# Optimization experiments

Measured on AMD Instinct MI355X. Metric: run time of the kernel, lower is better.

## Reference

```python
import jax, jax.numpy as jnp
import numpy as np

LMAX = 10
BATCH = 16384


def _pairs():
    return [(l1, l2) for l1 in range(LMAX + 1) for l2 in range(l1, LMAX + 1)]


def _cg_offsets():
    # flat-buffer offset and coupled dimension d=(2l1+1)(2l2+1) per (l1,l2) pair
    offs = {}
    off = 0
    for (l1, l2) in _pairs():
        d = (2 * l1 + 1) * (2 * l2 + 1)
        offs[(l1, l2)] = (off, d)
        off += d * d
    return offs, off


def _full_coeffs(coeffs):
    # coeffs: (B, LMAX+1, LMAX+1) complex, entry [:, l, m] holds f_{l,m} for m>=0.
    # Real-signal symmetry: f_{l,-m} = (-1)^m conj(f_{l,m}).
    f = {}
    for l in range(LMAX + 1):
        pos = coeffs[:, l, : l + 1]  # m = 0..l
        if l == 0:
            f[l] = pos
        else:
            mm = np.arange(l, 0, -1)  # |m| for m = -l..-1
            sign = jnp.asarray(((-1.0) ** mm), dtype=jnp.float32)
            neg = sign * jnp.conj(coeffs[:, l, 1 : l + 1][:, ::-1])
            f[l] = jnp.concatenate([neg, pos], axis=1)  # (B, 2l+1), m = -l..l
    return f


def setup_inputs() -> dict:
    key = jax.random.key(0)
    k1, k2, k3 = jax.random.split(key, 3)
    _, total = _cg_offsets()
    return {
        "coeffs_re": jax.random.normal(k1, (BATCH, LMAX + 1, LMAX + 1), dtype=jnp.float32),
        "coeffs_im": jax.random.normal(k2, (BATCH, LMAX + 1, LMAX + 1), dtype=jnp.float32),
        "cg_flat": jax.random.normal(k3, (total,), dtype=jnp.float32),
    }


def reference(coeffs_re, coeffs_im, cg_flat):
    coeffs = jax.lax.complex(coeffs_re, coeffs_im)  # (B, L+1, L+1) complex64
    f = _full_coeffs(coeffs)
    offs, _ = _cg_offsets()
    B = coeffs.shape[0]
    cols = []
    for (l1, l2) in _pairs():
        off, d = offs[(l1, l2)]
        cg = cg_flat[off : off + d * d].reshape(d, d).astype(coeffs.dtype)
        # tensor product of coefficient vectors, flattened: (B, (2l1+1)(2l2+1))
        tp = (f[l1][:, :, None] * f[l2][:, None, :]).reshape(B, d)
        transformed = tp @ cg  # (B, d)
        lmin = l2 - l1
        for l in range(lmin, min(l1 + l2, LMAX) + 1):
            s = l * l - lmin * lmin  # column offset of degree-l block in coupled basis
            blk = transformed[:, s : s + 2 * l + 1]
            cols.append(jnp.sum(blk * jnp.conj(f[l]), axis=-1))
    return jnp.stack(cols, axis=1)  # (B, 381) complex64
```

## Files before the change

### kernel.cpp

```cpp
#include <hip/hip_runtime.h>

#define LMAX   10
#define BATCH  16384
#define NCOLS  381
#define NF     121
#define NPAIRS 66

typedef __attribute__((ext_vector_type(8))) short    short8;
typedef __attribute__((ext_vector_type(8))) _Float16 half8;
typedef __attribute__((ext_vector_type(2))) _Float16 half2v;
typedef __attribute__((ext_vector_type(4))) float    floatx4;
typedef __attribute__((ext_vector_type(4))) unsigned uint4v;

__device__ __forceinline__ short f32_to_f16_bits(float x) {
    return __builtin_bit_cast(short, (_Float16)x);
}

__device__ const int kPairOrder[NPAIRS] = {
    65,64,63,62,61,60,58,59,56,57,55,52,53,54,49,51,47,50,48,46,
    43,44,41,42,40,45,36,34,39,37,35,27,33,38,29,25,26,28,32,18,
    19,24,30,31,15,16,17,20,22,23,14, 8, 9,10,21, 0, 1, 2, 3, 4,
     5, 6, 7,11,12,13
};

__device__ __forceinline__ void decode_pair_ext(int p, int& l1, int& l2,
                                                long long& off, int& colbase,
                                                int& c16off)
{
    long long o = 0; int cb = 0, c16 = 0, idx = 0;
    for (int a = 0; a <= LMAX; ++a) {
        for (int bq = a; bq <= LMAX; ++bq) {
            const int d    = (2*a+1)*(2*bq+1);
            const int lmin = bq - a;
            const int lmx  = (a + bq < LMAX) ? (a + bq) : LMAX;
            const int used = (lmx+1)*(lmx+1) - lmin*lmin;
            const int npan = (d + 31) >> 5;
            const int nt   = (used + 15) >> 4;
            if (idx == p) { l1 = a; l2 = bq; off = o; colbase = cb; c16off = c16; return; }
            o += (long long)d * d; cb += lmx - lmin + 1;
            c16 += nt * 16 * npan * 32; ++idx;
        }
    }
    l1 = l2 = 0; off = 0; colbase = 0; c16off = 0;
}

__global__ __launch_bounds__(256) void prep(const float* __restrict__ cre,
                                            const float* __restrict__ cim,
                                            const float* __restrict__ cg,
                                            float2* __restrict__ f,
                                            short* __restrict__ cg16)
{
    __shared__ __align__(16) char pbuf[30976];
    const int tid = threadIdx.x;

    if (blockIdx.x < 512) {
        float* sr = (float*)pbuf;
        float* si = sr + 32 * 121;
        const int btile = blockIdx.x * 32;
        for (int t = tid; t < 32 * 121; t += 256) {
            sr[t] = cre[(size_t)btile * 121 + t];
            si[t] = cim[(size_t)btile * 121 + t];
        }
        __syncthreads();
        for (int task = tid; task < 32 * 121; task += 256) {
            const int row = task & 31;
            const int idx = task >> 5;
            int l = (int)sqrtf((float)idx + 0.5f);
            if (l * l > idx) --l;
            if ((l + 1) * (l + 1) <= idx) ++l;
            const int m = idx - l * l - l;
            const float* crow  = sr + row * 121 + l * 11;
            const float* cirow = si + row * 121 + l * 11;
            float re, im;
            if (m >= 0) { re = crow[m]; im = cirow[m]; }
            else {
                const int a = -m;
                const float sg = (a & 1) ? -1.0f : 1.0f;
                re = sg * crow[a]; im = -sg * cirow[a];
            }
            f[(size_t)idx * BATCH + btile + row] = make_float2(re, im);
        }
        return;
    }

    const int bid2 = blockIdx.x - 512;
    const int pair = bid2 / 7;
    const int xk   = bid2 - pair * 7;

    int l1, l2, colbase, c16off; long long off;
    decode_pair_ext(pair, l1, l2, off, colbase, c16off);
    const int d    = (2*l1+1)*(2*l2+1);
    const int lmin = l2 - l1;
    const int lmx  = (l1 + l2 < LMAX) ? (l1 + l2) : LMAX;
    const int used = (lmx+1)*(lmx+1) - lmin*lmin;
    const int npan = (d + 31) >> 5;
    const int nt   = (used + 15) >> 4;
    const int K32  = npan * 32;
    const int kbase = xk * 64;
    if (kbase >= K32) return;
    const int kend  = (kbase + 64 < K32) ? kbase + 64 : K32;
    const int usedp = nt * 16;

    short* L = (short*)pbuf;

    {
        const int nn = tid & 127;
        const int kh = tid >> 7;
        for (int k = kbase + kh; k < kend; k += 2) {
            float v = 0.f;
            if (nn < used && k < d)
                v = cg[off + (size_t)k * d + nn];
            L[nn * 72 + (k - kbase)] = f32_to_f16_bits(v);
        }
    }
    __syncthreads();

    {
        const int oct = tid & 7;
        const int ng  = tid >> 3;
        const int kk  = kbase + oct * 8;
        if (kk < K32) {
            for (int nn = ng; nn < usedp; nn += 32) {
                const short8 vv = *(const short8*)&L[nn * 72 + oct * 8];
                *(short8*)(cg16 + (size_t)c16off + (size_t)nn * K32 + kk) = vv;
            }
        }
    }
}

template<int NT, bool BIGD2>
__device__ __forceinline__ void pair_body(const float2* __restrict__ f,
                                          const short* __restrict__ cg16,
                                          float* __restrict__ out,
                                          short* smem, int btile,
                                          int l1, int l2, int c16off, int colbase)
{
    const int d1 = 2*l1 + 1, d2 = 2*l2 + 1, d = d1 * d2;
    const int lmin = l2 - l1;
    const int lmx  = (l1 + l2 < LMAX) ? (l1 + l2) : LMAX;
    const int n_l  = lmx - lmin + 1;
    const int q1 = l1*l1, q2 = l2*l2;
    const int npan = (d + 31) >> 5;
    const int K32  = npan * 32;

    const int tid  = threadIdx.x;
    const int lane = tid & 63;
    const int w    = tid >> 6;
    const int quad = lane >> 4;
    const int r16  = lane & 15;

    constexpr int FS = 51;
    unsigned* f12 = (unsigned*)smem;
    short* B0 = smem + 64 * FS * 2;
    short* B1 = B0 + 128 * 32;

    {
        const int srow = tid & 63;
        unsigned* frw = f12 + srow * FS;
        const float2* f1p = f + (size_t)q1 * BATCH + btile + srow;
        const float2* f2p = f + (size_t)q2 * BATCH + btile + srow;
        for (int mm = tid >> 6; mm < FS; mm += 4) {
            float2 v;
            if (mm < d1) v = f1p[(size_t)mm * BATCH];
            else {
                int m2s = mm - d1;
                while (m2s >= d2) m2s -= d2;
                v = f2p[(size_t)m2s * BATCH];
            }
            half2v h; h.x = (_Float16)v.x; h.y = (_Float16)v.y;
            frw[mm] = __builtin_bit_cast(unsigned, h);
        }
    }

    const short* cgbase = cg16 + (size_t)c16off;
    const int nchunk = NT * 64;

    short8 pf0, pf1;
    const int ch0 = tid, ch1 = tid + 256;
    const int nr0 = ch0 >> 2, cc0 = ch0 & 3;
    const int nr1 = ch1 >> 2, cc1 = ch1 & 3;
    const size_t so0 = (size_t)nr0 * K32 + cc0 * 8;
    const size_t so1 = (size_t)nr1 * K32 + cc1 * 8;
    const int bo0 = nr0 * 32 + (((cc0 + (nr0 >> 1)) & 3) << 3);
    const int bo1 = nr1 * 32 + (((cc1 + (nr1 >> 1)) & 3) << 3);

    if (NT >= 4 || ch0 < nchunk) pf0 = *(const short8*)(cgbase + so0);
    if (NT >= 8 || ch1 < nchunk) pf1 = *(const short8*)(cgbase + so1);
    if (NT >= 4 || ch0 < nchunk) *(short8*)&B0[bo0] = pf0;
    if (NT >= 8 || ch1 < nchunk) *(short8*)&B0[bo1] = pf1;
    __syncthreads();

    floatx4 accR[NT], accI[NT];
#pragma unroll
    for (int i = 0; i < NT; ++i) {
        accR[i] = (floatx4)0.0f; accI[i] = (floatx4)0.0f;
    }

    const int arow = w * 16 + r16;
    const unsigned* frow = f12 + arow * FS;
    const int bswz = ((quad + (r16 >> 1)) & 3) << 3;

    const int k0q = quad * 8;
    int m1 = k0q / d2;
    int m2 = k0q - m1 * d2;
    const int q32 = 32 / d2;
    const int r32 = 32 - q32 * d2;

    for (int pan = 0; pan < npan; ++pan) {
        short* Bc = (pan & 1) ? B1 : B0;
        short* Bn = (pan & 1) ? B0 : B1;

        const bool more = (pan + 1) < npan;
        if (more) {
            const size_t kn = (size_t)(pan + 1) << 5;
            if (NT >= 4 || ch0 < nchunk) pf0 = *(const short8*)(cgbase + so0 + kn);
            if (NT >= 8 || ch1 < nchunk) pf1 = *(const short8*)(cgbase + so1 + kn);
        }

        unsigned ar[4], ai[4];
        {
            const unsigned* cb = frow + d1 + m2;
            if (BIGD2) {
                const unsigned a0 = frow[m1];
                const unsigned a1 = frow[m1 + 1];
                const int wpos = d2 - m2;
#pragma unroll
                for (int t = 0; t < 4; ++t) {
                    unsigned r01[2];
#pragma unroll
                    for (int u = 0; u < 2; ++u) {
                        const int j = 2*t + u;
                        const unsigned ad = (j >= wpos) ? a1 : a0;
                        const half2v a = __builtin_bit_cast(half2v, ad);
                        const half2v c = __builtin_bit_cast(half2v, cb[j]);
                        const _Float16 tr = a.x * c.x - a.y * c.y;
                        const _Float16 ti = a.x * c.y + a.y * c.x;
                        half2v rr; rr.x = tr; rr.y = ti;
                        r01[u] = __builtin_bit_cast(unsigned, rr);
                    }
                    ar[t] = (r01[0] & 0xffffu) | (r01[1] << 16);
                    ai[t] = (r01[0] >> 16)    | (r01[1] & 0xffff0000u);
                }
            } else {
                int mm1 = m1, tcnt = m2;
#pragma unroll
                for (int t = 0; t < 4; ++t) {
                    unsigned r01[2];
#pragma unroll
                    for (int u = 0; u < 2; ++u) {
                        const int j = 2*t + u;
                        const half2v a = __builtin_bit_cast(half2v, frow[mm1]);
                        const half2v c = __builtin_bit_cast(half2v, cb[j]);
                        const _Float16 tr = a.x * c.x - a.y * c.y;
                        const _Float16 ti = a.x * c.y + a.y * c.x;
                        half2v rr; rr.x = tr; rr.y = ti;
                        r01[u] = __builtin_bit_cast(unsigned, rr);
                        if (++tcnt == d2) { tcnt = 0; ++mm1; }
                    }
                    ar[t] = (r01[0] & 0xffffu) | (r01[1] << 16);
                    ai[t] = (r01[0] >> 16)    | (r01[1] & 0xffff0000u);
                }
            }
        }
        const half8 are = __builtin_bit_cast(half8, (uint4v){ar[0], ar[1], ar[2], ar[3]});
        const half8 aim = __builtin_bit_cast(half8, (uint4v){ai[0], ai[1], ai[2], ai[3]});

        m1 += q32; m2 += r32;
        if (m2 >= d2) { m2 -= d2; ++m1; }

#pragma unroll
        for (int n0 = 0; n0 < NT; ++n0) {
            const short8 b16 = *(const short8*)&Bc[(n0 * 16 + r16) * 32 + bswz];
            const half8 bb = __builtin_bit_cast(half8, b16);
            accR[n0] = __builtin_amdgcn_mfma_f32_16x16x32_f16(are, bb, accR[n0], 0, 0, 0);
            accI[n0] = __builtin_amdgcn_mfma_f32_16x16x32_f16(aim, bb, accI[n0], 0, 0, 0);
        }

        if (more) {
            if (NT >= 4 || ch0 < nchunk) *(short8*)&Bn[bo0] = pf0;
            if (NT >= 8 || ch1 < nchunk) *(short8*)&Bn[bo1] = pf1;
        }
        __syncthreads();
    }

    float* T = (float*)smem;
    const int ntask = 64 * n_l;
    float part[3] = {0.f, 0.f, 0.f};

#pragma unroll
    for (int n0 = 0; n0 < NT; ++n0)
#pragma unroll
        for (int r = 0; r < 4; ++r) {
            const int col = n0*16 + r16;
            if (col < 123)
                T[(w*16 + quad*4 + r) * 123 + col] = accR[n0][r];
        }
    __syncthreads();
    {
        int it = 0;
        for (int task = tid; task < ntask; task += 256, ++it) {
            const int trow = task & 63;
            const int li   = task >> 6;
            const int l    = lmin + li;
            const int sl   = l*l - lmin*lmin;
            const int W    = 2*l + 1;
            const float* Trow = T + trow * 123 + sl;
            const float2* fb = f + (size_t)(l*l) * BATCH + (btile + trow);
            float a0 = 0.f, a1 = 0.f;
#pragma unroll
            for (int j = 0; j < 21; j += 2) {
                const float  tv0 = (j < W) ? Trow[j] : 0.f;
                const float2 fv0 = fb[(size_t)j * BATCH];
                a0 = fmaf(tv0, fv0.x, a0);
                if (j + 1 < 21) {
                    const float  tv1 = (j + 1 < W) ? Trow[j + 1] : 0.f;
                    const float2 fv1 = fb[(size_t)(j + 1) * BATCH];
                    a1 = fmaf(tv1, fv1.x, a1);
                }
            }
            part[it] = a0 + a1;
        }
    }
    __syncthreads();

#pragma unroll
    for (int n0 = 0; n0 < NT; ++n0)
#pragma unroll
        for (int r = 0; r < 4; ++r) {
            const int col = n0*16 + r16;
            if (col < 123)
                T[(w*16 + quad*4 + r) * 123 + col] = accI[n0][r];
        }
    __syncthreads();
    {
        int it = 0;
        for (int task = tid; task < ntask; task += 256, ++it) {
            const int trow = task & 63;
            const int li   = task >> 6;
            const int l    = lmin + li;
            const int sl   = l*l - lmin*lmin;
            const int W    = 2*l + 1;
            const float* Trow = T + trow * 123 + sl;
            const float2* fb = f + (size_t)(l*l) * BATCH + (btile + trow);
            float a0 = part[it], a1 = 0.f;
#pragma unroll
            for (int j = 0; j < 21; j += 2) {
                const float  tv0 = (j < W) ? Trow[j] : 0.f;
                const float2 fv0 = fb[(size_t)j * BATCH];
                a0 = fmaf(tv0, fv0.y, a0);
                if (j + 1 < 21) {
                    const float  tv1 = (j + 1 < W) ? Trow[j + 1] : 0.f;
                    const float2 fv1 = fb[(size_t)(j + 1) * BATCH];
                    a1 = fmaf(tv1, fv1.y, a1);
                }
            }
            out[(size_t)(btile + trow) * NCOLS + colbase + li] = a0 + a1;
        }
    }
}

__global__ __launch_bounds__(256, 4) void so3_mfma(const float2* __restrict__ f,
                                                   const short* __restrict__ cg16,
                                                   float* __restrict__ out)
{
    __shared__ __align__(16) short smem[15744];
    const int btile = blockIdx.x * 64;
    const int p     = kPairOrder[blockIdx.y];
    int l1, l2, colbase, c16off; long long off;
    decode_pair_ext(p, l1, l2, off, colbase, c16off);
    const int lmin = l2 - l1;
    const int lmx  = (l1 + l2 < LMAX) ? (l1 + l2) : LMAX;
    const int used = (lmx+1)*(lmx+1) - lmin*lmin;
    const int nt   = (used + 15) >> 4;
    if (l2 >= 4) {
        switch (nt) {
            case 1: pair_body<1,true>(f, cg16, out, smem, btile, l1, l2, c16off, colbase); break;
            case 2: pair_body<2,true>(f, cg16, out, smem, btile, l1, l2, c16off, colbase); break;
            case 3: pair_body<3,true>(f, cg16, out, smem, btile, l1, l2, c16off, colbase); break;
            case 4: pair_body<4,true>(f, cg16, out, smem, btile, l1, l2, c16off, colbase); break;
            case 5: pair_body<5,true>(f, cg16, out, smem, btile, l1, l2, c16off, colbase); break;
            case 6: pair_body<6,true>(f, cg16, out, smem, btile, l1, l2, c16off, colbase); break;
            case 7: pair_body<7,true>(f, cg16, out, smem, btile, l1, l2, c16off, colbase); break;
            default: pair_body<8,true>(f, cg16, out, smem, btile, l1, l2, c16off, colbase); break;
        }
    } else {
        switch (nt) {
            case 1: pair_body<1,false>(f, cg16, out, smem, btile, l1, l2, c16off, colbase); break;
            case 2: pair_body<2,false>(f, cg16, out, smem, btile, l1, l2, c16off, colbase); break;
            case 3: pair_body<3,false>(f, cg16, out, smem, btile, l1, l2, c16off, colbase); break;
            default: pair_body<4,false>(f, cg16, out, smem, btile, l1, l2, c16off, colbase); break;
        }
    }
}

template<int L>
__device__ __forceinline__ float core_fb(const float2* f1v, const float2* f2v,
                                         const float2* flv,
                                         const float* __restrict__ cgp,
                                         int d1, int d2, int d)
{
    constexpr int W = 2*L + 1;
    float accr[W], acci[W];
#pragma unroll
    for (int k = 0; k < W; ++k) { accr[k] = 0.f; acci[k] = 0.f; }
    for (int m1 = 0; m1 < d1; ++m1) {
        const float2 a = f1v[m1];
        const float* rowbase = cgp + (size_t)m1 * d2 * d;
        for (int m2 = 0; m2 < d2; ++m2) {
            const float2 bb = f2v[m2];
            const float tr = a.x*bb.x - a.y*bb.y;
            const float ti = a.x*bb.y + a.y*bb.x;
            const float* row = rowbase + (size_t)m2 * d;
#pragma unroll
            for (int k = 0; k < W; ++k) {
                accr[k] = fmaf(tr, row[k], accr[k]);
                acci[k] = fmaf(ti, row[k], acci[k]);
            }
        }
    }
    float orr = 0.f;
#pragma unroll
    for (int k = 0; k < W; ++k)
        orr = fmaf(accr[k], flv[k].x, fmaf(acci[k], flv[k].y, orr));
    return orr;
}

__global__ __launch_bounds__(256) void so3_tp_direct(const float* __restrict__ cre,
                                                     const float* __restrict__ cim,
                                                     const float* __restrict__ cg,
                                                     float* __restrict__ out)
{
    const int b = blockIdx.x * blockDim.x + threadIdx.x;
    const int t = blockIdx.y;
    int l1 = 0, l2 = 0, l = 0; long long off = 0;
    {
        int tt = t; long long o = 0;
        bool found = false;
        for (int a = 0; a <= LMAX && !found; ++a)
            for (int bq = a; bq <= LMAX && !found; ++bq) {
                const int d = (2*a+1)*(2*bq+1);
                const int lmin = bq - a;
                const int lmx = (a+bq < LMAX) ? (a+bq) : LMAX;
                const int cnt = lmx - lmin + 1;
                if (tt < cnt) { l1 = a; l2 = bq; l = lmin + tt; off = o; found = true; }
                else { tt -= cnt; o += (long long)d*d; }
            }
    }
    const int d1 = 2*l1+1, d2 = 2*l2+1, d = d1*d2;
    const int lmin = l2 - l1;
    const int s = l*l - lmin*lmin;

    const float* cr = cre + (size_t)b * 121;
    const float* ci = cim + (size_t)b * 121;
    float2 f1v[21], f2v[21], flv[21];
    for (int j = 0; j <= 2*l1; ++j) {
        const int m = j - l1;
        if (m >= 0) f1v[j] = make_float2(cr[l1*11+m], ci[l1*11+m]);
        else { const int a2 = -m; const float sg = (a2&1)?-1.f:1.f;
               f1v[j] = make_float2(sg*cr[l1*11+a2], -sg*ci[l1*11+a2]); }
    }
    for (int j = 0; j <= 2*l2; ++j) {
        const int m = j - l2;
        if (m >= 0) f2v[j] = make_float2(cr[l2*11+m], ci[l2*11+m]);
        else { const int a2 = -m; const float sg = (a2&1)?-1.f:1.f;
               f2v[j] = make_float2(sg*cr[l2*11+a2], -sg*ci[l2*11+a2]); }
    }
    for (int j = 0; j <= 2*l; ++j) {
        const int m = j - l;
        if (m >= 0) flv[j] = make_float2(cr[l*11+m], ci[l*11+m]);
        else { const int a2 = -m; const float sg = (a2&1)?-1.f:1.f;
               flv[j] = make_float2(sg*cr[l*11+a2], -sg*ci[l*11+a2]); }
    }
    const float* cgp = cg + off + s;
    float r;
    switch (l) {
        case 0: r = core_fb<0>(f1v,f2v,flv,cgp,d1,d2,d); break;
        case 1: r = core_fb<1>(f1v,f2v,flv,cgp,d1,d2,d); break;
        case 2: r = core_fb<2>(f1v,f2v,flv,cgp,d1,d2,d); break;
        case 3: r = core_fb<3>(f1v,f2v,flv,cgp,d1,d2,d); break;
        case 4: r = core_fb<4>(f1v,f2v,flv,cgp,d1,d2,d); break;
        case 5: r = core_fb<5>(f1v,f2v,flv,cgp,d1,d2,d); break;
        case 6: r = core_fb<6>(f1v,f2v,flv,cgp,d1,d2,d); break;
        case 7: r = core_fb<7>(f1v,f2v,flv,cgp,d1,d2,d); break;
        case 8: r = core_fb<8>(f1v,f2v,flv,cgp,d1,d2,d); break;
        case 9: r = core_fb<9>(f1v,f2v,flv,cgp,d1,d2,d); break;
        default: r = core_fb<10>(f1v,f2v,flv,cgp,d1,d2,d); break;
    }
    out[(size_t)b * NCOLS + t] = r;
}

extern "C" void kernel_launch(void* const* d_in, const int* in_sizes, int n_in,
                              void* d_out, int out_size, void* d_ws, size_t ws_size,
                              hipStream_t stream)
{
    const float* cre = (const float*)d_in[0];
    const float* cim = (const float*)d_in[1];
    const float* cg  = (const float*)d_in[2];
    float* out = (float*)d_out;

    long long c16_total = 0;
    for (int l1 = 0; l1 <= LMAX; ++l1)
        for (int l2 = l1; l2 <= LMAX; ++l2) {
            const int d    = (2*l1+1)*(2*l2+1);
            const int lmin = l2 - l1;
            const int lmx  = (l1 + l2 < LMAX) ? (l1 + l2) : LMAX;
            const int used = (lmx+1)*(lmx+1) - lmin*lmin;
            c16_total += (long long)((used+15)/16) * 16 * ((d+31)/32) * 32;
        }

    const size_t f_bytes = (size_t)NF * BATCH * sizeof(float2);
    const size_t need    = f_bytes + (size_t)c16_total * 2;

    if (ws_size >= need) {
        float2* f    = (float2*)d_ws;
        short*  cg16 = (short*)((char*)d_ws + f_bytes);
        prep    <<<dim3(512 + 7 * NPAIRS), 256, 0, stream>>>(cre, cim, cg, f, cg16);
        so3_mfma<<<dim3(BATCH/64, NPAIRS), 256, 0, stream>>>(f, cg16, out);
    } else {
        so3_tp_direct<<<dim3(BATCH/256, NCOLS), 256, 0, stream>>>(cre, cim, cg, out);
    }
}
```

Measured before the change: 341.3 us.

## Double batch tile to 128 rows with 512-thread blocks sharing CG panels

Each block now handles 128 batch rows with 8 waves instead of 64 rows with 4 waves, so every CG panel loaded into shared memory feeds twice as many rows. This halves the global CG traffic and the number of blocks. The epilogue is split into two halves that reuse the same staging buffer, which adds extra barriers. Shared memory per block grows and the larger blocks may reduce occupancy and hurt load balance across the grid.

```diff
diff --git a/kernel.cpp b/kernel.cpp
--- a/kernel.cpp
+++ b/kernel.cpp
@@ -151,15 +151,15 @@
 
     constexpr int FS = 51;
     unsigned* f12 = (unsigned*)smem;
-    short* B0 = smem + 64 * FS * 2;
+    short* B0 = smem + 128 * FS * 2;
     short* B1 = B0 + 128 * 32;
 
     {
-        const int srow = tid & 63;
+        const int srow = tid & 127;
         unsigned* frw = f12 + srow * FS;
         const float2* f1p = f + (size_t)q1 * BATCH + btile + srow;
         const float2* f2p = f + (size_t)q2 * BATCH + btile + srow;
-        for (int mm = tid >> 6; mm < FS; mm += 4) {
+        for (int mm = tid >> 7; mm < FS; mm += 4) {
             float2 v;
             if (mm < d1) v = f1p[(size_t)mm * BATCH];
             else {
@@ -173,21 +173,17 @@
     }
 
     const short* cgbase = cg16 + (size_t)c16off;
-    const int nchunk = NT * 64;
-
-    short8 pf0, pf1;
-    const int ch0 = tid, ch1 = tid + 256;
-    const int nr0 = ch0 >> 2, cc0 = ch0 & 3;
-    const int nr1 = ch1 >> 2, cc1 = ch1 & 3;
-    const size_t so0 = (size_t)nr0 * K32 + cc0 * 8;
-    const size_t so1 = (size_t)nr1 * K32 + cc1 * 8;
-    const int bo0 = nr0 * 32 + (((cc0 + (nr0 >> 1)) & 3) << 3);
-    const int bo1 = nr1 * 32 + (((cc1 + (nr1 >> 1)) & 3) << 3);
-
-    if (NT >= 4 || ch0 < nchunk) pf0 = *(const short8*)(cgbase + so0);
-    if (NT >= 8 || ch1 < nchunk) pf1 = *(const short8*)(cgbase + so1);
-    if (NT >= 4 || ch0 < nchunk) *(short8*)&B0[bo0] = pf0;
-    if (NT >= 8 || ch1 < nchunk) *(short8*)&B0[bo1] = pf1;
+
+    short8 pf;
+    const int nr = tid >> 2, cc = tid & 3;
+    const size_t so = (size_t)nr * K32 + cc * 8;
+    const int bo = nr * 32 + (((cc + (nr >> 1)) & 3) << 3);
+    const bool act = (NT >= 8) || (tid < NT * 64);
+
+    if (act) {
+        pf = *(const short8*)(cgbase + so);
+        *(short8*)&B0[bo] = pf;
+    }
     __syncthreads();
 
     floatx4 accR[NT], accI[NT];
@@ -211,11 +207,8 @@
         short* Bn = (pan & 1) ? B0 : B1;
 
         const bool more = (pan + 1) < npan;
-        if (more) {
-            const size_t kn = (size_t)(pan + 1) << 5;
-            if (NT >= 4 || ch0 < nchunk) pf0 = *(const short8*)(cgbase + so0 + kn);
-            if (NT >= 8 || ch1 < nchunk) pf1 = *(const short8*)(cgbase + so1 + kn);
-        }
+        if (more && act)
+            pf = *(const short8*)(cgbase + so + ((size_t)(pan + 1) << 5));
 
         unsigned ar[4], ai[4];
         {
@@ -276,95 +269,104 @@
             accI[n0] = __builtin_amdgcn_mfma_f32_16x16x32_f16(aim, bb, accI[n0], 0, 0, 0);
         }
 
-        if (more) {
-            if (NT >= 4 || ch0 < nchunk) *(short8*)&Bn[bo0] = pf0;
-            if (NT >= 8 || ch1 < nchunk) *(short8*)&Bn[bo1] = pf1;
-        }
+        if (more && act)
+            *(short8*)&Bn[bo] = pf;
         __syncthreads();
     }
 
     float* T = (float*)smem;
     const int ntask = 64 * n_l;
-    float part[3] = {0.f, 0.f, 0.f};
-
-#pragma unroll
-    for (int n0 = 0; n0 < NT; ++n0)
-#pragma unroll
-        for (int r = 0; r < 4; ++r) {
-            const int col = n0*16 + r16;
-            if (col < 123)
-                T[(w*16 + quad*4 + r) * 123 + col] = accR[n0][r];
-        }
-    __syncthreads();
-    {
-        int it = 0;
-        for (int task = tid; task < ntask; task += 256, ++it) {
-            const int trow = task & 63;
-            const int li   = task >> 6;
-            const int l    = lmin + li;
-            const int sl   = l*l - lmin*lmin;
-            const int W    = 2*l + 1;
-            const float* Trow = T + trow * 123 + sl;
-            const float2* fb = f + (size_t)(l*l) * BATCH + (btile + trow);
-            float a0 = 0.f, a1 = 0.f;
-#pragma unroll
-            for (int j = 0; j < 21; j += 2) {
-                const float  tv0 = (j < W) ? Trow[j] : 0.f;
-                const float2 fv0 = fb[(size_t)j * BATCH];
-                a0 = fmaf(tv0, fv0.x, a0);
-                if (j + 1 < 21) {
-                    const float  tv1 = (j + 1 < W) ? Trow[j + 1] : 0.f;
-                    const float2 fv1 = fb[(size_t)(j + 1) * BATCH];
-                    a1 = fmaf(tv1, fv1.x, a1);
+    const int hw   = w >> 2;
+    const int rloc = (w & 3) * 16 + quad * 4;
+
+#pragma unroll 1
+    for (int h = 0; h < 2; ++h) {
+        float part[2] = {0.f, 0.f};
+        if (hw == h) {
+#pragma unroll
+            for (int n0 = 0; n0 < NT; ++n0) {
+                const int col = n0*16 + r16;
+                if (col < 123) {
+#pragma unroll
+                    for (int r = 0; r < 4; ++r)
+                        T[(rloc + r) * 123 + col] = accR[n0][r];
                 }
             }
-            part[it] = a0 + a1;
-        }
-    }
-    __syncthreads();
-
-#pragma unroll
-    for (int n0 = 0; n0 < NT; ++n0)
-#pragma unroll
-        for (int r = 0; r < 4; ++r) {
-            const int col = n0*16 + r16;
-            if (col < 123)
-                T[(w*16 + quad*4 + r) * 123 + col] = accI[n0][r];
-        }
-    __syncthreads();
-    {
-        int it = 0;
-        for (int task = tid; task < ntask; task += 256, ++it) {
-            const int trow = task & 63;
-            const int li   = task >> 6;
-            const int l    = lmin + li;
-            const int sl   = l*l - lmin*lmin;
-            const int W    = 2*l + 1;
-            const float* Trow = T + trow * 123 + sl;
-            const float2* fb = f + (size_t)(l*l) * BATCH + (btile + trow);
-            float a0 = part[it], a1 = 0.f;
-#pragma unroll
-            for (int j = 0; j < 21; j += 2) {
-                const float  tv0 = (j < W) ? Trow[j] : 0.f;
-                const float2 fv0 = fb[(size_t)j * BATCH];
-                a0 = fmaf(tv0, fv0.y, a0);
-                if (j + 1 < 21) {
-                    const float  tv1 = (j + 1 < W) ? Trow[j + 1] : 0.f;
-                    const float2 fv1 = fb[(size_t)(j + 1) * BATCH];
-                    a1 = fmaf(tv1, fv1.y, a1);
+        }
+        __syncthreads();
+        {
+            int it = 0;
+            for (int task = tid; task < ntask; task += 512, ++it) {
+                const int trow = task & 63;
+                const int li   = task >> 6;
+                const int l    = lmin + li;
+                const int sl   = l*l - lmin*lmin;
+                const int W    = 2*l + 1;
+                const float* Trow = T + trow * 123 + sl;
+                const float2* fb = f + (size_t)(l*l) * BATCH + (btile + h*64 + trow);
+                float a0 = 0.f, a1 = 0.f;
+#pragma unroll
+                for (int j = 0; j < 21; j += 2) {
+                    const float  tv0 = (j < W) ? Trow[j] : 0.f;
+                    const float2 fv0 = fb[(size_t)j * BATCH];
+                    a0 = fmaf(tv0, fv0.x, a0);
+                    if (j + 1 < 21) {
+                        const float  tv1 = (j + 1 < W) ? Trow[j + 1] : 0.f;
+                        const float2 fv1 = fb[(size_t)(j + 1) * BATCH];
+                        a1 = fmaf(tv1, fv1.x, a1);
+                    }
                 }
-            }
-            out[(size_t)(btile + trow) * NCOLS + colbase + li] = a0 + a1;
-        }
-    }
-}
-
-__global__ __launch_bounds__(256, 4) void so3_mfma(const float2* __restrict__ f,
+                part[it] = a0 + a1;
+            }
+        }
+        __syncthreads();
+        if (hw == h) {
+#pragma unroll
+            for (int n0 = 0; n0 < NT; ++n0) {
+                const int col = n0*16 + r16;
+                if (col < 123) {
+#pragma unroll
+                    for (int r = 0; r < 4; ++r)
+                        T[(rloc + r) * 123 + col] = accI[n0][r];
+                }
+            }
+        }
+        __syncthreads();
+        {
+            int it = 0;
+            for (int task = tid; task < ntask; task += 512, ++it) {
+                const int trow = task & 63;
+                const int li   = task >> 6;
+                const int l    = lmin + li;
+                const int sl   = l*l - lmin*lmin;
+                const int W    = 2*l + 1;
+                const float* Trow = T + trow * 123 + sl;
+                const float2* fb = f + (size_t)(l*l) * BATCH + (btile + h*64 + trow);
+                float a0 = part[it], a1 = 0.f;
+#pragma unroll
+                for (int j = 0; j < 21; j += 2) {
+                    const float  tv0 = (j < W) ? Trow[j] : 0.f;
+                    const float2 fv0 = fb[(size_t)j * BATCH];
+                    a0 = fmaf(tv0, fv0.y, a0);
+                    if (j + 1 < 21) {
+                        const float  tv1 = (j + 1 < W) ? Trow[j + 1] : 0.f;
+                        const float2 fv1 = fb[(size_t)(j + 1) * BATCH];
+                        a1 = fmaf(tv1, fv1.y, a1);
+                    }
+                }
+                out[(size_t)(btile + h*64 + trow) * NCOLS + colbase + li] = a0 + a1;
+            }
+        }
+        if (h == 0) __syncthreads();
+    }
+}
+
+__global__ __launch_bounds__(512, 4) void so3_mfma(const float2* __restrict__ f,
                                                    const short* __restrict__ cg16,
                                                    float* __restrict__ out)
 {
-    __shared__ __align__(16) short smem[15744];
-    const int btile = blockIdx.x * 64;
+    __shared__ __align__(16) short smem[21248];
+    const int btile = blockIdx.x * 128;
     const int p     = kPairOrder[blockIdx.y];
     int l1, l2, colbase, c16off; long long off;
     decode_pair_ext(p, l1, l2, off, colbase, c16off);
@@ -515,7 +517,7 @@
         float2* f    = (float2*)d_ws;
         short*  cg16 = (short*)((char*)d_ws + f_bytes);
         prep    <<<dim3(512 + 7 * NPAIRS), 256, 0, stream>>>(cre, cim, cg, f, cg16);
-        so3_mfma<<<dim3(BATCH/64, NPAIRS), 256, 0, stream>>>(f, cg16, out);
+        so3_mfma<<<dim3(BATCH/128, NPAIRS), 512, 0, stream>>>(f, cg16, out);
     } else {
         so3_tp_direct<<<dim3(BATCH/256, NCOLS), 256, 0, stream>>>(cre, cim, cg, out);
     }
```

Result: slower. 465.4 us (+36.3%).

## Process two K-panels per barrier with double-width prefetch buffers

Applied to the files above, without the earlier changes.

The MFMA main loop now handles two 32-wide K panels per iteration and prefetches two panels of CG coefficients into doubled LDS buffers. This halves the number of __syncthreads barriers per pair and gives more loads in flight to cover global latency. In exchange, LDS per block grows and launch bounds drop from 4 to 3 blocks per CU. That cuts occupancy and adds register pressure from the extra prefetch registers.

```diff
diff --git a/kernel.cpp b/kernel.cpp
--- a/kernel.cpp
+++ b/kernel.cpp
@@ -152,7 +152,7 @@
     constexpr int FS = 51;
     unsigned* f12 = (unsigned*)smem;
     short* B0 = smem + 64 * FS * 2;
-    short* B1 = B0 + 128 * 32;
+    short* B1 = B0 + 8192;
 
     {
         const int srow = tid & 63;
@@ -175,7 +175,7 @@
     const short* cgbase = cg16 + (size_t)c16off;
     const int nchunk = NT * 64;
 
-    short8 pf0, pf1;
+    short8 pfa0, pfa1, pfb0, pfb1;
     const int ch0 = tid, ch1 = tid + 256;
     const int nr0 = ch0 >> 2, cc0 = ch0 & 3;
     const int nr1 = ch1 >> 2, cc1 = ch1 & 3;
@@ -184,10 +184,16 @@
     const int bo0 = nr0 * 32 + (((cc0 + (nr0 >> 1)) & 3) << 3);
     const int bo1 = nr1 * 32 + (((cc1 + (nr1 >> 1)) & 3) << 3);
 
-    if (NT >= 4 || ch0 < nchunk) pf0 = *(const short8*)(cgbase + so0);
-    if (NT >= 8 || ch1 < nchunk) pf1 = *(const short8*)(cgbase + so1);
-    if (NT >= 4 || ch0 < nchunk) *(short8*)&B0[bo0] = pf0;
-    if (NT >= 8 || ch1 < nchunk) *(short8*)&B0[bo1] = pf1;
+    if (NT >= 4 || ch0 < nchunk) { pfa0 = *(const short8*)(cgbase + so0);
+                                   *(short8*)&B0[bo0] = pfa0; }
+    if (NT >= 8 || ch1 < nchunk) { pfa1 = *(const short8*)(cgbase + so1);
+                                   *(short8*)&B0[bo1] = pfa1; }
+    if (npan > 1) {
+        if (NT >= 4 || ch0 < nchunk) { pfb0 = *(const short8*)(cgbase + so0 + 32);
+                                       *(short8*)&B0[4096 + bo0] = pfb0; }
+        if (NT >= 8 || ch1 < nchunk) { pfb1 = *(const short8*)(cgbase + so1 + 32);
+                                       *(short8*)&B0[4096 + bo1] = pfb1; }
+    }
     __syncthreads();
 
     floatx4 accR[NT], accI[NT];
@@ -206,79 +212,96 @@
     const int q32 = 32 / d2;
     const int r32 = 32 - q32 * d2;
 
-    for (int pan = 0; pan < npan; ++pan) {
-        short* Bc = (pan & 1) ? B1 : B0;
-        short* Bn = (pan & 1) ? B0 : B1;
-
-        const bool more = (pan + 1) < npan;
-        if (more) {
-            const size_t kn = (size_t)(pan + 1) << 5;
-            if (NT >= 4 || ch0 < nchunk) pf0 = *(const short8*)(cgbase + so0 + kn);
-            if (NT >= 8 || ch1 < nchunk) pf1 = *(const short8*)(cgbase + so1 + kn);
-        }
-
-        unsigned ar[4], ai[4];
-        {
-            const unsigned* cb = frow + d1 + m2;
-            if (BIGD2) {
-                const unsigned a0 = frow[m1];
-                const unsigned a1 = frow[m1 + 1];
-                const int wpos = d2 - m2;
-#pragma unroll
-                for (int t = 0; t < 4; ++t) {
-                    unsigned r01[2];
-#pragma unroll
-                    for (int u = 0; u < 2; ++u) {
-                        const int j = 2*t + u;
-                        const unsigned ad = (j >= wpos) ? a1 : a0;
-                        const half2v a = __builtin_bit_cast(half2v, ad);
-                        const half2v c = __builtin_bit_cast(half2v, cb[j]);
-                        const _Float16 tr = a.x * c.x - a.y * c.y;
-                        const _Float16 ti = a.x * c.y + a.y * c.x;
-                        half2v rr; rr.x = tr; rr.y = ti;
-                        r01[u] = __builtin_bit_cast(unsigned, rr);
+    const int nslot = (npan + 1) >> 1;
+    for (int s = 0; s < nslot; ++s) {
+        short* Bc = (s & 1) ? B1 : B0;
+        short* Bn = (s & 1) ? B0 : B1;
+
+        const bool morea = (2*s + 2) < npan;
+        const bool moreb = (2*s + 3) < npan;
+        if (morea) {
+            const size_t kn = (size_t)(2*s + 2) << 5;
+            if (NT >= 4 || ch0 < nchunk) pfa0 = *(const short8*)(cgbase + so0 + kn);
+            if (NT >= 8 || ch1 < nchunk) pfa1 = *(const short8*)(cgbase + so1 + kn);
+        }
+        if (moreb) {
+            const size_t kn = (size_t)(2*s + 3) << 5;
+            if (NT >= 4 || ch0 < nchunk) pfb0 = *(const short8*)(cgbase + so0 + kn);
+            if (NT >= 8 || ch1 < nchunk) pfb1 = *(const short8*)(cgbase + so1 + kn);
+        }
+
+#pragma unroll
+        for (int pp = 0; pp < 2; ++pp) {
+            if (pp == 0 || (2*s + 1) < npan) {
+                unsigned ar[4], ai[4];
+                {
+                    const unsigned* cb = frow + d1 + m2;
+                    if (BIGD2) {
+                        const unsigned a0 = frow[m1];
+                        const unsigned a1 = frow[m1 + 1];
+                        const int wpos = d2 - m2;
+#pragma unroll
+                        for (int t = 0; t < 4; ++t) {
+                            unsigned r01[2];
+#pragma unroll
+                            for (int u = 0; u < 2; ++u) {
+                                const int j = 2*t + u;
+                                const unsigned ad = (j >= wpos) ? a1 : a0;
+                                const half2v a = __builtin_bit_cast(half2v, ad);
+                                const half2v c = __builtin_bit_cast(half2v, cb[j]);
+                                const _Float16 tr = a.x * c.x - a.y * c.y;
+                                const _Float16 ti = a.x * c.y + a.y * c.x;
+                                half2v rr; rr.x = tr; rr.y = ti;
+                                r01[u] = __builtin_bit_cast(unsigned, rr);
+                            }
+                            ar[t] = (r01[0] & 0xffffu) | (r01[1] << 16);
+                            ai[t] = (r01[0] >> 16)    | (r01[1] & 0xffff0000u);
+                        }
+                    } else {
+                        int mm1 = m1, tcnt = m2;
+#pragma unroll
+                        for (int t = 0; t < 4; ++t) {
+                            unsigned r01[2];
+#pragma unroll
+                            for (int u = 0; u < 2; ++u) {
+                                const int j = 2*t + u;
+                                const half2v a = __builtin_bit_cast(half2v, frow[mm1]);
+                                const half2v c = __builtin_bit_cast(half2v, cb[j]);
+                                const _Float16 tr = a.x * c.x - a.y * c.y;
+                                const _Float16 ti = a.x * c.y + a.y * c.x;
+                                half2v rr; rr.x = tr; rr.y = ti;
+                                r01[u] = __builtin_bit_cast(unsigned, rr);
+                                if (++tcnt == d2) { tcnt = 0; ++mm1; }
+                            }
+                            ar[t] = (r01[0] & 0xffffu) | (r01[1] << 16);
+                            ai[t] = (r01[0] >> 16)    | (r01[1] & 0xffff0000u);
+                        }
                     }
-                    ar[t] = (r01[0] & 0xffffu) | (r01[1] << 16);
-                    ai[t] = (r01[0] >> 16)    | (r01[1] & 0xffff0000u);
                 }
-            } else {
-                int mm1 = m1, tcnt = m2;
-#pragma unroll
-                for (int t = 0; t < 4; ++t) {
-                    unsigned r01[2];
-#pragma unroll
-                    for (int u = 0; u < 2; ++u) {
-                        const int j = 2*t + u;
-                        const half2v a = __builtin_bit_cast(half2v, frow[mm1]);
-                        const half2v c = __builtin_bit_cast(half2v, cb[j]);
-                        const _Float16 tr = a.x * c.x - a.y * c.y;
-                        const _Float16 ti = a.x * c.y + a.y * c.x;
-                        half2v rr; rr.x = tr; rr.y = ti;
-                        r01[u] = __builtin_bit_cast(unsigned, rr);
-                        if (++tcnt == d2) { tcnt = 0; ++mm1; }
-                    }
-                    ar[t] = (r01[0] & 0xffffu) | (r01[1] << 16);
-                    ai[t] = (r01[0] >> 16)    | (r01[1] & 0xffff0000u);
+                const half8 are = __builtin_bit_cast(half8, (uint4v){ar[0], ar[1], ar[2], ar[3]});
+                const half8 aim = __builtin_bit_cast(half8, (uint4v){ai[0], ai[1], ai[2], ai[3]});
+
+                m1 += q32; m2 += r32;
+                if (m2 >= d2) { m2 -= d2; ++m1; }
+
+                const short* Bp = Bc + pp * 4096;
+#pragma unroll
+                for (int n0 = 0; n0 < NT; ++n0) {
+                    const short8 b16 = *(const short8*)&Bp[(n0 * 16 + r16) * 32 + bswz];
+                    const half8 bb = __builtin_bit_cast(half8, b16);
+                    accR[n0] = __builtin_amdgcn_mfma_f32_16x16x32_f16(are, bb, accR[n0], 0, 0, 0);
+                    accI[n0] = __builtin_amdgcn_mfma_f32_16x16x32_f16(aim, bb, accI[n0], 0, 0, 0);
                 }
             }
         }
-        const half8 are = __builtin_bit_cast(half8, (uint4v){ar[0], ar[1], ar[2], ar[3]});
-        const half8 aim = __builtin_bit_cast(half8, (uint4v){ai[0], ai[1], ai[2], ai[3]});
-
-        m1 += q32; m2 += r32;
-        if (m2 >= d2) { m2 -= d2; ++m1; }
-
-#pragma unroll
-        for (int n0 = 0; n0 < NT; ++n0) {
-            const short8 b16 = *(const short8*)&Bc[(n0 * 16 + r16) * 32 + bswz];
-            const half8 bb = __builtin_bit_cast(half8, b16);
-            accR[n0] = __builtin_amdgcn_mfma_f32_16x16x32_f16(are, bb, accR[n0], 0, 0, 0);
-            accI[n0] = __builtin_amdgcn_mfma_f32_16x16x32_f16(aim, bb, accI[n0], 0, 0, 0);
-        }
-
-        if (more) {
-            if (NT >= 4 || ch0 < nchunk) *(short8*)&Bn[bo0] = pf0;
-            if (NT >= 8 || ch1 < nchunk) *(short8*)&Bn[bo1] = pf1;
+
+        if (morea) {
+            if (NT >= 4 || ch0 < nchunk) *(short8*)&Bn[bo0] = pfa0;
+            if (NT >= 8 || ch1 < nchunk) *(short8*)&Bn[bo1] = pfa1;
+        }
+        if (moreb) {
+            if (NT >= 4 || ch0 < nchunk) *(short8*)&Bn[4096 + bo0] = pfb0;
+            if (NT >= 8 || ch1 < nchunk) *(short8*)&Bn[4096 + bo1] = pfb1;
         }
         __syncthreads();
     }
@@ -359,11 +382,11 @@
     }
 }
 
-__global__ __launch_bounds__(256, 4) void so3_mfma(const float2* __restrict__ f,
+__global__ __launch_bounds__(256, 3) void so3_mfma(const float2* __restrict__ f,
                                                    const short* __restrict__ cg16,
                                                    float* __restrict__ out)
 {
-    __shared__ __align__(16) short smem[15744];
+    __shared__ __align__(16) short smem[22912];
     const int btile = blockIdx.x * 64;
     const int p     = kPairOrder[blockIdx.y];
     int l1, l2, colbase, c16off; long long off;
```

Measured after the change: 394.9 us. 15.7% more time.
